# Optimization experiments

Hardware: AMD Instinct MI355X
Metric: run time of the kernel (lower is better)

Reference implementation:

```python
import jax, jax.numpy as jnp
import numpy as np

N, D, E, TOP_K = 65536, 2048, 8, 2


def setup_inputs() -> dict:
    key = jax.random.key(0)
    k1, k2 = jax.random.split(key)
    x = jax.random.normal(k1, (N, D), dtype=jnp.float32)
    # router linear params (nn.Linear(input_dim, expert_num))
    W = jax.random.normal(k2, (E, D), dtype=jnp.float32) * (1.0 / np.sqrt(D))
    b = jnp.zeros((E,), dtype=jnp.float32)
    return {"x": x, "W": W, "b": b}


def reference(x, W, b):
    # gating_logits = softmax(Linear(x))  -> [N, E]
    logits = jnp.einsum("nd,ed->ne", x, W) + b
    gate = jax.nn.softmax(logits, axis=-1)
    # top-k expert selection (torch.topk equivalent)
    top_k_vals, top_k_idx = jax.lax.top_k(gate, TOP_K)  # [N, k], [N, k]
    # Expert.forward is a stub in the source and the original forward
    # returns x unchanged; we return the realized routing quantities + x.
    return top_k_vals, top_k_idx, x
```

## Files before the change

kernel.cpp:

```cpp
#include <hip/hip_runtime.h>
#include <hip/hip_bf16.h>

#define N_ROWS 65536
#define DIM    2048
#define NEXP   8
#define TOPK   2
#define RPW    2
#define CHUNKS (DIM / (64 * 4))
#define BLOCK  1024
#define GRID   512

typedef float f4 __attribute__((ext_vector_type(4)));

__global__ __launch_bounds__(BLOCK, 4) void moe_router_kernel(
    const float* __restrict__ x,
    const float* __restrict__ W,
    const float* __restrict__ b,
    float* __restrict__ out_vals,
    float* __restrict__ out_idx,
    float* __restrict__ out_x)
{
    __shared__ float sW[NEXP * DIM];

    const f4* W4 = (const f4*)W;
    f4* sW4 = (f4*)sW;
    for (int i = threadIdx.x; i < NEXP * DIM / 4; i += BLOCK)
        sW4[i] = W4[i];
    __syncthreads();

    const int lane   = threadIdx.x & 63;
    const int wave   = (int)((blockIdx.x * BLOCK + threadIdx.x) >> 6);
    const int nwaves = (GRID * BLOCK) >> 6;

    const f4* x4 = (const f4*)x;
    f4* ox4 = (f4*)out_x;
    const int row_f4 = DIM / 4;

    for (int g = wave; g < N_ROWS / RPW; g += nwaves) {
        const int row0 = g * RPW;

        float acc[RPW][NEXP];
#pragma unroll
        for (int r = 0; r < RPW; ++r)
#pragma unroll
            for (int e = 0; e < NEXP; ++e) acc[r][e] = 0.0f;

#pragma unroll 2
        for (int c = 0; c < CHUNKS; ++c) {
            const int d4 = c * 64 + lane;
            f4 xv[RPW];
#pragma unroll
            for (int r = 0; r < RPW; ++r) {
                const size_t off = (size_t)(row0 + r) * row_f4 + d4;
                xv[r] = x4[off];
                ox4[off] = xv[r];
            }
#pragma unroll
            for (int e = 0; e < NEXP; ++e) {
                const f4 wv = sW4[e * row_f4 + d4];
#pragma unroll
                for (int r = 0; r < RPW; ++r) {
                    acc[r][e] += xv[r].x * wv.x;
                    acc[r][e] += xv[r].y * wv.y;
                    acc[r][e] += xv[r].z * wv.z;
                    acc[r][e] += xv[r].w * wv.w;
                }
            }
        }

#pragma unroll
        for (int r = 0; r < RPW; ++r) {
#pragma unroll
            for (int e = 0; e < NEXP; ++e) {
                float v = acc[r][e];
                v += __shfl_xor(v, 32, 64);
                v += __shfl_xor(v, 16, 64);
                v += __shfl_xor(v, 8, 64);
                v += __shfl_xor(v, 4, 64);
                v += __shfl_xor(v, 2, 64);
                v += __shfl_xor(v, 1, 64);
                acc[r][e] = v;
            }
        }

        if (lane < RPW) {
            const int r = lane;
            float lg[NEXP];
#pragma unroll
            for (int e = 0; e < NEXP; ++e) lg[e] = acc[r][e] + b[e];

            float mx = lg[0];
#pragma unroll
            for (int e = 1; e < NEXP; ++e) mx = fmaxf(mx, lg[e]);

            float p[NEXP];
            float sum = 0.0f;
#pragma unroll
            for (int e = 0; e < NEXP; ++e) { p[e] = __expf(lg[e] - mx); sum += p[e]; }
            const float inv = 1.0f / sum;

            int i1 = 0;
#pragma unroll
            for (int e = 1; e < NEXP; ++e) if (lg[e] > lg[i1]) i1 = e;
            int i2 = (i1 == 0) ? 1 : 0;
#pragma unroll
            for (int e = 0; e < NEXP; ++e)
                if (e != i1 && e != i2 && lg[e] > lg[i2]) i2 = e;

            const int row = row0 + r;
            out_vals[row * 2 + 0] = p[i1] * inv;
            out_vals[row * 2 + 1] = p[i2] * inv;
            out_idx[row * 2 + 0]  = (float)i1;
            out_idx[row * 2 + 1]  = (float)i2;
        }
    }
}

extern "C" void kernel_launch(void* const* d_in, const int* in_sizes, int n_in,
                              void* d_out, int out_size, void* d_ws, size_t ws_size,
                              hipStream_t stream) {
    const float* x = (const float*)d_in[0];
    const float* W = (const float*)d_in[1];
    const float* b = (const float*)d_in[2];

    float* out = (float*)d_out;
    float* out_vals = out;
    float* out_idx  = out + (size_t)N_ROWS * 2;
    float* out_x    = out + (size_t)N_ROWS * 4;

    moe_router_kernel<<<GRID, BLOCK, 0, stream>>>(x, W, b, out_vals, out_idx, out_x);
}
```

Measured before the change: 223.6 us.

## Process one row per wave with register double-buffered x prefetch

Switches from two rows per wave to one row per wave and loads the next 128 float4 columns of x before computing on the current ones, so global loads overlap the copy-out and dot products. The launch-bounds occupancy hint rises from 4 to 8. This aims to hide load latency in a bandwidth-bound kernel. The trade-offs are possible register pressure from the tighter bound and fewer independent accumulators per wave.

Result: slower. 848.3 us (+279.5%).

```diff
diff --git a/kernel.cpp b/kernel.cpp
--- a/kernel.cpp
+++ b/kernel.cpp
@@ -5,14 +5,13 @@
 #define DIM    2048
 #define NEXP   8
 #define TOPK   2
-#define RPW    2
-#define CHUNKS (DIM / (64 * 4))
+#define STEPS  4
 #define BLOCK  1024
 #define GRID   512
 
 typedef float f4 __attribute__((ext_vector_type(4)));
 
-__global__ __launch_bounds__(BLOCK, 4) void moe_router_kernel(
+__global__ __launch_bounds__(BLOCK, 8) void moe_router_kernel(
     const float* __restrict__ x,
     const float* __restrict__ W,
     const float* __restrict__ b,
@@ -36,58 +35,57 @@
     f4* ox4 = (f4*)out_x;
     const int row_f4 = DIM / 4;
 
-    for (int g = wave; g < N_ROWS / RPW; g += nwaves) {
-        const int row0 = g * RPW;
+    for (int row = wave; row < N_ROWS; row += nwaves) {
+        const size_t base = (size_t)row * row_f4 + lane;
 
-        float acc[RPW][NEXP];
+        float acc[NEXP];
 #pragma unroll
-        for (int r = 0; r < RPW; ++r)
-#pragma unroll
-            for (int e = 0; e < NEXP; ++e) acc[r][e] = 0.0f;
+        for (int e = 0; e < NEXP; ++e) acc[e] = 0.0f;
+
+        f4 x0 = x4[base];
+        f4 x1 = x4[base + 64];
 
 #pragma unroll 2
-        for (int c = 0; c < CHUNKS; ++c) {
-            const int d4 = c * 64 + lane;
-            f4 xv[RPW];
-#pragma unroll
-            for (int r = 0; r < RPW; ++r) {
-                const size_t off = (size_t)(row0 + r) * row_f4 + d4;
-                xv[r] = x4[off];
-                ox4[off] = xv[r];
+        for (int s = 0; s < STEPS; ++s) {
+            const int col = s * 128;
+
+            f4 n0, n1;
+            if (s + 1 < STEPS) {
+                n0 = x4[base + col + 128];
+                n1 = x4[base + col + 192];
             }
+
+            ox4[base + col]      = x0;
+            ox4[base + col + 64] = x1;
+
 #pragma unroll
             for (int e = 0; e < NEXP; ++e) {
-                const f4 wv = sW4[e * row_f4 + d4];
-#pragma unroll
-                for (int r = 0; r < RPW; ++r) {
-                    acc[r][e] += xv[r].x * wv.x;
-                    acc[r][e] += xv[r].y * wv.y;
-                    acc[r][e] += xv[r].z * wv.z;
-                    acc[r][e] += xv[r].w * wv.w;
-                }
+                const f4 w0 = sW4[e * row_f4 + col + lane];
+                const f4 w1 = sW4[e * row_f4 + col + 64 + lane];
+                acc[e] += x0.x * w0.x + x0.y * w0.y + x0.z * w0.z + x0.w * w0.w
+                        + x1.x * w1.x + x1.y * w1.y + x1.z * w1.z + x1.w * w1.w;
             }
+
+            x0 = n0;
+            x1 = n1;
         }
 
 #pragma unroll
-        for (int r = 0; r < RPW; ++r) {
-#pragma unroll
-            for (int e = 0; e < NEXP; ++e) {
-                float v = acc[r][e];
-                v += __shfl_xor(v, 32, 64);
-                v += __shfl_xor(v, 16, 64);
-                v += __shfl_xor(v, 8, 64);
-                v += __shfl_xor(v, 4, 64);
-                v += __shfl_xor(v, 2, 64);
-                v += __shfl_xor(v, 1, 64);
-                acc[r][e] = v;
-            }
+        for (int e = 0; e < NEXP; ++e) {
+            float v = acc[e];
+            v += __shfl_xor(v, 32, 64);
+            v += __shfl_xor(v, 16, 64);
+            v += __shfl_xor(v, 8, 64);
+            v += __shfl_xor(v, 4, 64);
+            v += __shfl_xor(v, 2, 64);
+            v += __shfl_xor(v, 1, 64);
+            acc[e] = v;
         }
 
-        if (lane < RPW) {
-            const int r = lane;
+        if (lane == 0) {
             float lg[NEXP];
 #pragma unroll
-            for (int e = 0; e < NEXP; ++e) lg[e] = acc[r][e] + b[e];
+            for (int e = 0; e < NEXP; ++e) lg[e] = acc[e] + b[e];
 
             float mx = lg[0];
 #pragma unroll
@@ -107,7 +105,6 @@
             for (int e = 0; e < NEXP; ++e)
                 if (e != i1 && e != i2 && lg[e] > lg[i2]) i2 = e;
 
-            const int row = row0 + r;
             out_vals[row * 2 + 0] = p[i1] * inv;
             out_vals[row * 2 + 1] = p[i2] * inv;
             out_idx[row * 2 + 0]  = (float)i1;
```
